# Kernel optimization log

Hardware: AMD Instinct MI355X
Metric: run time of the kernel (lower is better)

Reference implementation:

```python
import jax, jax.numpy as jnp
import numpy as np

NUM_HEADS = 4
B, C, N = 2, 128, 4096
NS = N // 2


def setup_inputs() -> dict:
    key = jax.random.key(0)
    ks = jax.random.split(key, 10)
    # idx_select/idx_drop together form a permutation of [0, N) per batch
    perms = jax.vmap(lambda k: jax.random.permutation(k, N))(jax.random.split(ks[8], B))
    idx_select = perms[:, :NS][:, None, :].astype(jnp.int64)
    idx_drop = perms[:, NS:][:, None, :].astype(jnp.int64)
    return {
        "pcd_up": jax.random.normal(ks[0], (B, C, N), jnp.float32),
        "points_select": jax.random.normal(ks[1], (B, C, NS), jnp.float32),
        "points_drop": jax.random.normal(ks[2], (B, C, NS), jnp.float32),
        "pcd_up_xyz": jax.random.normal(ks[3], (B, 3, N), jnp.float32),
        "Wq": jax.random.normal(ks[4], (C, C), jnp.float32) * 0.05,
        "Wk": jax.random.normal(ks[5], (C, C), jnp.float32) * 0.05,
        "Wv": jax.random.normal(ks[6], (C, C), jnp.float32) * 0.05,
        "Wskip": jax.random.normal(ks[7], (C, C), jnp.float32) * 0.05,
        "idx_select": idx_select,
        "idx_drop": idx_drop,
    }


def _concat_by_idx(a, b, idx_a, idx_b):
    # torch: target.scatter(-1, idx, cat([a,b],-1)) with idx expanded over channels
    src = jnp.concatenate([a, b], axis=-1)                  # [B, C, N]
    idx = jnp.concatenate([idx_a, idx_b], axis=-1)[:, 0, :]  # [B, N]
    return jax.vmap(lambda s, i: jnp.zeros_like(s).at[:, i].set(s))(src, idx)


def reference(pcd_up, points_select, points_drop, pcd_up_xyz, Wq, Wk, Wv, Wskip,
              idx_select, idx_drop):
    x = _concat_by_idx(points_select, points_drop, idx_select, idx_drop)  # [B,C,N]
    b, _, n = x.shape

    def proj_split(W, xx):
        y = jnp.einsum('oc,bcn->bon', W, xx)  # 1x1 Conv1d, no bias
        return y.reshape(b, NUM_HEADS, y.shape[1] // NUM_HEADS, n)  # [B,H,D,N]

    q = proj_split(Wq, x)
    k = proj_split(Wk, x)
    v = proj_split(Wv, x)
    dq = q.shape[2]
    # energy = q^T @ k, scaled by sqrt(q_depth)
    energy = jnp.einsum('bhdn,bhdm->bhnm', q, k) / jnp.sqrt(jnp.asarray(dq, x.dtype))
    attn = jax.nn.softmax(energy, axis=-1)                   # [B,H,N,N]
    out = jnp.einsum('bhnm,bhdm->bhnd', attn, v)             # [B,H,N,Dv]
    out = out.transpose(0, 2, 1, 3).reshape(b, n, -1).transpose(0, 2, 1)  # [B,v_out,N]
    return out + jnp.einsum('oc,bcn->bon', Wskip, pcd_up)
```

## Files before the change

### kernel.cpp

```cpp
#include <hip/hip_runtime.h>
#include <cstdint>

#define B_ 2
#define C_ 128
#define N_ 4096
#define H_ 4
#define D_ 32

typedef unsigned short ushort_t;
typedef __attribute__((ext_vector_type(8))) short bf16x8;
typedef __attribute__((ext_vector_type(4))) float f32x4;
typedef __attribute__((ext_vector_type(4))) unsigned int u32x4;

__device__ __forceinline__ ushort_t f2bf(float f) {
  unsigned int u = __builtin_bit_cast(unsigned int, f);
  u += 0x7fffu + ((u >> 16) & 1u);
  return (ushort_t)(u >> 16);
}

__device__ __forceinline__ void stage16(const ushort_t* g, ushort_t* l) {
  __builtin_amdgcn_global_load_lds(
      (const __attribute__((address_space(1))) unsigned int*)g,
      (__attribute__((address_space(3))) unsigned int*)l, 16, 0, 0);
}

__global__ __launch_bounds__(256) void k_prep(const float* __restrict__ psel,
                                              const float* __restrict__ pdrop,
                                              const int* __restrict__ isel,
                                              const int* __restrict__ idrop,
                                              const float* __restrict__ Wq,
                                              const float* __restrict__ Wk,
                                              const float* __restrict__ Wv,
                                              const float* __restrict__ Wsk,
                                              ushort_t* __restrict__ xT,
                                              ushort_t* __restrict__ Wb) {
  int z = blockIdx.z;
  int b = blockIdx.y;
  int t = threadIdx.x;
  {
    int gid = (((z * 2 + b) * 64 + blockIdx.x) << 8) + t;
    int m = gid >> 14, e = gid & 16383;
    const float* src = (m == 0) ? Wq : (m == 1) ? Wk : (m == 2) ? Wv : Wsk;
    float sc = (m == 0) ? 0.25506552f : 1.0f;
    Wb[m * 16384 + e] = f2bf(src[e] * sc);
  }
  const float* src = z ? pdrop : psel;
  const int* idx = z ? idrop : isel;
  __shared__ ushort_t tile[128][34];
  int i0 = blockIdx.x * 32;
  {
    int c = t >> 1, ih = (t & 1) * 16;
    const float4* p = (const float4*)(src + ((size_t)(b * 128 + c) * 2048 + i0 + ih));
#pragma unroll
    for (int g = 0; g < 4; ++g) {
      float4 v = p[g];
      tile[c][ih + g * 4 + 0] = f2bf(v.x);
      tile[c][ih + g * 4 + 1] = f2bf(v.y);
      tile[c][ih + g * 4 + 2] = f2bf(v.z);
      tile[c][ih + g * 4 + 3] = f2bf(v.w);
    }
  }
  __syncthreads();
  {
    int i = t >> 3, c0 = (t & 7) * 16;
    int n = idx[b * 2048 + i0 + i];
    alignas(16) ushort_t outv[16];
#pragma unroll
    for (int j = 0; j < 16; ++j) outv[j] = tile[c0 + j][i];
    uint4* q = (uint4*)(xT + ((size_t)(b * 4096 + n) * 128 + c0));
    q[0] = *(uint4*)outv; q[1] = *(uint4*)(outv + 8);
  }
}

__global__ __launch_bounds__(256) void k_proj(const ushort_t* __restrict__ xT,
                                              const ushort_t* __restrict__ Wb,
                                              ushort_t* __restrict__ Kb,
                                              ushort_t* __restrict__ Vt) {
  __shared__ float y[128][66];
  int n0 = blockIdx.x * 64, wt = blockIdx.y, b = blockIdx.z, t = threadIdx.x;
  int wave = t >> 6, lane = t & 63, lr = lane & 15, quad = lane >> 4;
  const ushort_t* W = Wb + (size_t)(wt + 1) * 16384;

  f32x4 acc[2][4];
#pragma unroll
  for (int mt = 0; mt < 2; ++mt)
#pragma unroll
    for (int nt = 0; nt < 4; ++nt) acc[mt][nt] = (f32x4){0.f, 0.f, 0.f, 0.f};
#pragma unroll
  for (int kc = 0; kc < 128; kc += 32) {
    bf16x8 a[2], bb[4];
#pragma unroll
    for (int mt = 0; mt < 2; ++mt)
      a[mt] = *(const bf16x8*)(W + (size_t)(wave * 32 + mt * 16 + lr) * 128 + kc + quad * 8);
#pragma unroll
    for (int nt = 0; nt < 4; ++nt)
      bb[nt] = *(const bf16x8*)(xT + ((size_t)(b * 4096 + n0 + nt * 16 + lr)) * 128 + kc + quad * 8);
#pragma unroll
    for (int mt = 0; mt < 2; ++mt)
#pragma unroll
      for (int nt = 0; nt < 4; ++nt)
        acc[mt][nt] = __builtin_amdgcn_mfma_f32_16x16x32_bf16(a[mt], bb[nt], acc[mt][nt], 0, 0, 0);
  }

#pragma unroll
  for (int mt = 0; mt < 2; ++mt)
#pragma unroll
    for (int nt = 0; nt < 4; ++nt)
#pragma unroll
      for (int r = 0; r < 4; ++r)
        y[wave * 32 + mt * 16 + quad * 4 + r][nt * 16 + lr] = acc[mt][nt][r];
  __syncthreads();

  if (wt == 0) {
    int n = t >> 2, dq = (t & 3) * 8;
#pragma unroll
    for (int h = 0; h < 4; ++h) {
      alignas(16) ushort_t vals[8];
#pragma unroll
      for (int j = 0; j < 8; ++j) vals[j] = f2bf(y[h * 32 + dq + j][n]);
      *(uint4*)(Kb + (((size_t)(b * 4 + h) * 4096 + n0 + n) * 32 + dq)) = *(uint4*)vals;
    }
  } else {
    int o = t >> 1, half = t & 1;
    int h = o >> 5, d = o & 31;
    alignas(16) ushort_t vals[32];
#pragma unroll
    for (int j = 0; j < 32; ++j) {
      int c = half * 32 + ((j >> 3) * 4 + (j & 3) + ((j & 4) << 2));
      vals[j] = f2bf(y[o][c]);
    }
    uint4* dst = (uint4*)(Vt + ((size_t)(b * 4 + h) * 32 + d) * 4096 + n0 + half * 32);
#pragma unroll
    for (int g = 0; g < 4; ++g) dst[g] = *(uint4*)(vals + g * 8);
  }
}

__global__ __launch_bounds__(1024) void k_attn(const ushort_t* __restrict__ xT,
                                               const float* __restrict__ pcd,
                                               const ushort_t* __restrict__ Wb,
                                               const ushort_t* __restrict__ Kb,
                                               const ushort_t* __restrict__ Vt,
                                               float* __restrict__ outp) {
  __shared__ ushort_t qT[4][32 * 40];
  __shared__ ushort_t stg[4][2][8192];

  int bh = blockIdx.x & 7;
  int q0 = (blockIdx.x >> 3) * 128;
  int b = bh >> 2, h = bh & 3;
  int t = threadIdx.x, wave = t >> 6, lane = t & 63, lr = lane & 15, quad = lane >> 4;
  int qh = wave & 3, kq = wave >> 2, lw = qh;
  int qbase = q0 + qh * 32;
  const ushort_t* xb = xT + (size_t)b * N_ * 128;
  const ushort_t* wqp = Wb + (size_t)h * 32 * 128;
  const ushort_t* Kp = Kb + (size_t)bh * N_ * 32;
  const ushort_t* Vp = Vt + (size_t)bh * 32 * N_;
  const int ks = kq * 1024;

#define STAGE_CHUNK(kcn, buf)                                                          \
  {                                                                                    \
    ushort_t* kb_ = stg[kq][buf];                                                      \
    ushort_t* vb_ = kb_ + 4096;                                                        \
    _Pragma("unroll") for (int j = 0; j < 2; ++j) {                                    \
      int s = lw * 2 + j;                                                              \
      stage16(Kp + (size_t)((kcn) + (s & 1) * 64 + lane) * 32 + (s >> 1) * 8,          \
              kb_ + s * 512);                                                          \
      int I = s * 64 + lane;                                                           \
      stage16(Vp + (size_t)(I & 31) * N_ + (kcn) + ((I >> 5) * 8), vb_ + s * 512);     \
    }                                                                                  \
  }

  if (kq == 0) {
    f32x4 accq[2][2];
#pragma unroll
    for (int mt = 0; mt < 2; ++mt)
#pragma unroll
      for (int nt = 0; nt < 2; ++nt) accq[mt][nt] = (f32x4){0.f, 0.f, 0.f, 0.f};
#pragma unroll
    for (int kc = 0; kc < 128; kc += 32) {
      bf16x8 ax[2], bw[2];
#pragma unroll
      for (int mt = 0; mt < 2; ++mt)
        ax[mt] = *(const bf16x8*)(xb + (size_t)(qbase + mt * 16 + lr) * 128 + kc + quad * 8);
#pragma unroll
      for (int nt = 0; nt < 2; ++nt)
        bw[nt] = *(const bf16x8*)(wqp + (size_t)(nt * 16 + lr) * 128 + kc + quad * 8);
#pragma unroll
      for (int mt = 0; mt < 2; ++mt)
#pragma unroll
        for (int nt = 0; nt < 2; ++nt)
          accq[mt][nt] = __builtin_amdgcn_mfma_f32_16x16x32_bf16(ax[mt], bw[nt], accq[mt][nt], 0, 0, 0);
    }
#pragma unroll
    for (int mt = 0; mt < 2; ++mt)
#pragma unroll
      for (int nt = 0; nt < 2; ++nt)
#pragma unroll
        for (int r = 0; r < 4; ++r)
          qT[qh][(mt * 16 + quad * 4 + r) * 40 + nt * 16 + lr] = f2bf(accq[mt][nt][r]);
  }

  STAGE_CHUNK(ks, 0);

  f32x4 accS[2][2];
#pragma unroll
  for (int mt = 0; mt < 2; ++mt)
#pragma unroll
    for (int nt = 0; nt < 2; ++nt) accS[mt][nt] = (f32x4){0.f, 0.f, 0.f, 0.f};
  if (kq == 1) {
    const ushort_t* wsk = Wb + 3 * 16384 + (size_t)h * 32 * 128;
#pragma unroll
    for (int kc = 0; kc < 128; kc += 32) {
      bf16x8 aS[2], bW[2];
#pragma unroll
      for (int mt = 0; mt < 2; ++mt) {
        alignas(16) ushort_t tmp[8];
#pragma unroll
        for (int j = 0; j < 8; ++j)
          tmp[j] = f2bf(pcd[((size_t)(b * 128 + kc + quad * 8 + j)) * 4096 + qbase + mt * 16 + lr]);
        aS[mt] = *(bf16x8*)tmp;
      }
#pragma unroll
      for (int nt = 0; nt < 2; ++nt)
        bW[nt] = *(const bf16x8*)(wsk + (size_t)(nt * 16 + lr) * 128 + kc + quad * 8);
#pragma unroll
      for (int mt = 0; mt < 2; ++mt)
#pragma unroll
        for (int nt = 0; nt < 2; ++nt)
          accS[mt][nt] = __builtin_amdgcn_mfma_f32_16x16x32_bf16(aS[mt], bW[nt], accS[mt][nt], 0, 0, 0);
    }
  }
  __syncthreads();

  bf16x8 aq0 = *(const bf16x8*)(&qT[qh][lr * 40 + quad * 8]);
  bf16x8 aq1 = *(const bf16x8*)(&qT[qh][(16 + lr) * 40 + quad * 8]);

  bf16x8 vones;
#pragma unroll
  for (int j = 0; j < 8; ++j) vones[j] = (short)0x3F80;

  f32x4 accO[2][2];
  f32x4 accR[2];
#pragma unroll
  for (int qf = 0; qf < 2; ++qf) {
#pragma unroll
    for (int dt = 0; dt < 2; ++dt) accO[qf][dt] = (f32x4){0.f, 0.f, 0.f, 0.f};
    accR[qf] = (f32x4){0.f, 0.f, 0.f, 0.f};
  }

  for (int it = 0; it < 8; ++it) {
    int cur = it & 1;
    if (it + 1 < 8) STAGE_CHUNK(ks + (it + 1) * 128, cur ^ 1);
    const ushort_t* kb = stg[kq][cur];
    const ushort_t* vb = kb + 4096;
#pragma unroll
    for (int g = 0; g < 4; ++g) {
      bf16x8 bk0 = *(const bf16x8*)(kb + (quad * 128 + g * 32 + lr) * 8);
      bf16x8 bk1 = *(const bf16x8*)(kb + (quad * 128 + g * 32 + 16 + lr) * 8);
      bf16x8 bv0 = *(const bf16x8*)(vb + ((g * 4 + quad) * 32 + lr) * 8);
      bf16x8 bv1 = *(const bf16x8*)(vb + ((g * 4 + quad) * 32 + 16 + lr) * 8);

      f32x4 z = {0.f, 0.f, 0.f, 0.f};
      f32x4 s0 = __builtin_amdgcn_mfma_f32_16x16x32_bf16(bk0, aq0, z, 0, 0, 0);
      f32x4 s1 = __builtin_amdgcn_mfma_f32_16x16x32_bf16(bk1, aq0, z, 0, 0, 0);
      f32x4 s2 = __builtin_amdgcn_mfma_f32_16x16x32_bf16(bk0, aq1, z, 0, 0, 0);
      f32x4 s3 = __builtin_amdgcn_mfma_f32_16x16x32_bf16(bk1, aq1, z, 0, 0, 0);
      float p0[4], p1[4], p2[4], p3[4];
#pragma unroll
      for (int r = 0; r < 4; ++r) {
        p0[r] = __builtin_amdgcn_exp2f(s0[r]);
        p1[r] = __builtin_amdgcn_exp2f(s1[r]);
        p2[r] = __builtin_amdgcn_exp2f(s2[r]);
        p3[r] = __builtin_amdgcn_exp2f(s3[r]);
      }
      u32x4 pk0, pk1;
      pk0.x = __builtin_amdgcn_perm(__builtin_bit_cast(unsigned int, p0[1]),
                                    __builtin_bit_cast(unsigned int, p0[0]), 0x07060302u);
      pk0.y = __builtin_amdgcn_perm(__builtin_bit_cast(unsigned int, p0[3]),
                                    __builtin_bit_cast(unsigned int, p0[2]), 0x07060302u);
      pk0.z = __builtin_amdgcn_perm(__builtin_bit_cast(unsigned int, p1[1]),
                                    __builtin_bit_cast(unsigned int, p1[0]), 0x07060302u);
      pk0.w = __builtin_amdgcn_perm(__builtin_bit_cast(unsigned int, p1[3]),
                                    __builtin_bit_cast(unsigned int, p1[2]), 0x07060302u);
      pk1.x = __builtin_amdgcn_perm(__builtin_bit_cast(unsigned int, p2[1]),
                                    __builtin_bit_cast(unsigned int, p2[0]), 0x07060302u);
      pk1.y = __builtin_amdgcn_perm(__builtin_bit_cast(unsigned int, p2[3]),
                                    __builtin_bit_cast(unsigned int, p2[2]), 0x07060302u);
      pk1.z = __builtin_amdgcn_perm(__builtin_bit_cast(unsigned int, p3[1]),
                                    __builtin_bit_cast(unsigned int, p3[0]), 0x07060302u);
      pk1.w = __builtin_amdgcn_perm(__builtin_bit_cast(unsigned int, p3[3]),
                                    __builtin_bit_cast(unsigned int, p3[2]), 0x07060302u);
      bf16x8 ap0 = __builtin_bit_cast(bf16x8, pk0);
      bf16x8 ap1 = __builtin_bit_cast(bf16x8, pk1);
      accO[0][0] = __builtin_amdgcn_mfma_f32_16x16x32_bf16(ap0, bv0, accO[0][0], 0, 0, 0);
      accO[0][1] = __builtin_amdgcn_mfma_f32_16x16x32_bf16(ap0, bv1, accO[0][1], 0, 0, 0);
      accO[1][0] = __builtin_amdgcn_mfma_f32_16x16x32_bf16(ap1, bv0, accO[1][0], 0, 0, 0);
      accO[1][1] = __builtin_amdgcn_mfma_f32_16x16x32_bf16(ap1, bv1, accO[1][1], 0, 0, 0);
      accR[0] = __builtin_amdgcn_mfma_f32_16x16x32_bf16(ap0, vones, accR[0], 0, 0, 0);
      accR[1] = __builtin_amdgcn_mfma_f32_16x16x32_bf16(ap1, vones, accR[1], 0, 0, 0);
    }
    __syncthreads();
  }

  float* pbuf = (float*)&stg[0][0][0];
  float* skipbuf = pbuf + 18432;
  float* obuf = pbuf + 22528;

  if (kq != 0) {
    float* pb = pbuf + (((kq - 1) * 4 + qh) * 64 + lane) * 24;
#pragma unroll
    for (int qf = 0; qf < 2; ++qf) {
#pragma unroll
      for (int dt = 0; dt < 2; ++dt)
#pragma unroll
        for (int r = 0; r < 4; ++r) pb[qf * 8 + dt * 4 + r] = accO[qf][dt][r];
#pragma unroll
      for (int r = 0; r < 4; ++r) pb[16 + qf * 4 + r] = accR[qf][r];
    }
    if (kq == 1) {
      float* sb = skipbuf + (qh * 64 + lane) * 16;
#pragma unroll
      for (int qf = 0; qf < 2; ++qf)
#pragma unroll
        for (int dt = 0; dt < 2; ++dt)
#pragma unroll
          for (int r = 0; r < 4; ++r) sb[qf * 8 + dt * 4 + r] = accS[qf][dt][r];
    }
  }
  __syncthreads();
  if (kq != 0) return;

#pragma unroll
  for (int j = 0; j < 3; ++j) {
    const float* pb = pbuf + ((j * 4 + qh) * 64 + lane) * 24;
#pragma unroll
    for (int qf = 0; qf < 2; ++qf) {
#pragma unroll
      for (int dt = 0; dt < 2; ++dt)
#pragma unroll
        for (int r = 0; r < 4; ++r) accO[qf][dt][r] += pb[qf * 8 + dt * 4 + r];
#pragma unroll
      for (int r = 0; r < 4; ++r) accR[qf][r] += pb[16 + qf * 4 + r];
    }
  }

  const float* sb = skipbuf + (qh * 64 + lane) * 16;
  float* ob = obuf + qh * 32 * 33;
#pragma unroll
  for (int qf = 0; qf < 2; ++qf) {
    float rinv[4];
#pragma unroll
    for (int r = 0; r < 4; ++r) rinv[r] = 1.0f / accR[qf][r];
#pragma unroll
    for (int dt = 0; dt < 2; ++dt)
#pragma unroll
      for (int r = 0; r < 4; ++r)
        ob[(dt * 16 + lr) * 33 + qf * 16 + quad * 4 + r] =
            accO[qf][dt][r] * rinv[r] + sb[qf * 8 + dt * 4 + r];
  }

  int d = lane >> 1, q16 = (lane & 1) * 16;
  float* po = outp + ((size_t)(b * 128 + h * 32 + d)) * N_ + qbase + q16;
#pragma unroll
  for (int g = 0; g < 4; ++g) {
    float4 r0;
    r0.x = ob[d * 33 + q16 + g * 4 + 0];
    r0.y = ob[d * 33 + q16 + g * 4 + 1];
    r0.z = ob[d * 33 + q16 + g * 4 + 2];
    r0.w = ob[d * 33 + q16 + g * 4 + 3];
    *(float4*)(po + g * 4) = r0;
  }
}

extern "C" void kernel_launch(void* const* d_in, const int* in_sizes, int n_in,
                              void* d_out, int out_size, void* d_ws, size_t ws_size,
                              hipStream_t stream) {
  const float* pcd_up = (const float*)d_in[0];
  const float* psel   = (const float*)d_in[1];
  const float* pdrop  = (const float*)d_in[2];
  const float* Wq  = (const float*)d_in[4];
  const float* Wk  = (const float*)d_in[5];
  const float* Wv  = (const float*)d_in[6];
  const float* Wsk = (const float*)d_in[7];
  const int* isel  = (const int*)d_in[8];
  const int* idrop = (const int*)d_in[9];
  float* out = (float*)d_out;

  ushort_t* xT = (ushort_t*)d_ws;
  ushort_t* Wb = xT + 1048576;
  ushort_t* Kb = Wb + 65536;
  ushort_t* Vt = Kb + 1048576;

  hipLaunchKernelGGL(k_prep, dim3(64, 2, 2), dim3(256), 0, stream,
                     psel, pdrop, isel, idrop, Wq, Wk, Wv, Wsk, xT, Wb);
  hipLaunchKernelGGL(k_proj, dim3(64, 2, 2), dim3(256), 0, stream, xT, Wb, Kb, Vt);
  hipLaunchKernelGGL(k_attn, dim3(256), dim3(1024), 0, stream,
                     xT, pcd_up, Wb, Kb, Vt, out);
}
```

Measured before the change: 113.4 us.

## Use per-wave private K/V staging and drop block-wide barriers in the attention loop

Before, each group of four query waves cooperatively staged 128-key K/V chunks into shared LDS and hit a block-wide __syncthreads every iteration. Now every wave stages its own 32-key chunk into a private double buffer and relies only on an s_waitcnt vmcnt wait, so waves no longer block one another. The loop runs 32 smaller iterations instead of 8. In exchange, the four waves with the same key range each fetch the same K/V data, raising global/L2 load traffic fourfold. The last iteration also issues a wrapped, unused prefetch.

```diff
diff --git a/kernel.cpp b/kernel.cpp
--- a/kernel.cpp
+++ b/kernel.cpp
@@ -142,31 +142,30 @@
                                                const ushort_t* __restrict__ Vt,
                                                float* __restrict__ outp) {
   __shared__ ushort_t qT[4][32 * 40];
-  __shared__ ushort_t stg[4][2][8192];
+  __shared__ ushort_t stg[16][2][2048];
 
   int bh = blockIdx.x & 7;
   int q0 = (blockIdx.x >> 3) * 128;
   int b = bh >> 2, h = bh & 3;
   int t = threadIdx.x, wave = t >> 6, lane = t & 63, lr = lane & 15, quad = lane >> 4;
-  int qh = wave & 3, kq = wave >> 2, lw = qh;
+  int qh = wave & 3, kq = wave >> 2;
   int qbase = q0 + qh * 32;
   const ushort_t* xb = xT + (size_t)b * N_ * 128;
   const ushort_t* wqp = Wb + (size_t)h * 32 * 128;
   const ushort_t* Kp = Kb + (size_t)bh * N_ * 32;
   const ushort_t* Vp = Vt + (size_t)bh * 32 * N_;
   const int ks = kq * 1024;
-
-#define STAGE_CHUNK(kcn, buf)                                                          \
-  {                                                                                    \
-    ushort_t* kb_ = stg[kq][buf];                                                      \
-    ushort_t* vb_ = kb_ + 4096;                                                        \
-    _Pragma("unroll") for (int j = 0; j < 2; ++j) {                                    \
-      int s = lw * 2 + j;                                                              \
-      stage16(Kp + (size_t)((kcn) + (s & 1) * 64 + lane) * 32 + (s >> 1) * 8,          \
-              kb_ + s * 512);                                                          \
-      int I = s * 64 + lane;                                                           \
-      stage16(Vp + (size_t)(I & 31) * N_ + (kcn) + ((I >> 5) * 8), vb_ + s * 512);     \
-    }                                                                                  \
+  int lk = lane & 31, lh = lane >> 5;
+
+#define STAGE_CHUNK(kcn, buf)                                                     \
+  {                                                                               \
+    ushort_t* kb_ = stg[wave][buf];                                               \
+    ushort_t* vb_ = kb_ + 1024;                                                   \
+    _Pragma("unroll") for (int s = 0; s < 2; ++s) {                               \
+      stage16(Kp + (size_t)((kcn) + lk) * 32 + (s * 2 + lh) * 8, kb_ + s * 512);  \
+      stage16(Vp + (size_t)lk * (size_t)N_ + (kcn) + (s * 2 + lh) * 8,            \
+              vb_ + s * 512);                                                     \
+    }                                                                             \
   }
 
   if (kq == 0) {
@@ -198,8 +197,6 @@
         for (int r = 0; r < 4; ++r)
           qT[qh][(mt * 16 + quad * 4 + r) * 40 + nt * 16 + lr] = f2bf(accq[mt][nt][r]);
   }
-
-  STAGE_CHUNK(ks, 0);
 
   f32x4 accS[2][2];
 #pragma unroll
@@ -229,6 +226,8 @@
           accS[mt][nt] = __builtin_amdgcn_mfma_f32_16x16x32_bf16(aS[mt], bW[nt], accS[mt][nt], 0, 0, 0);
     }
   }
+
+  STAGE_CHUNK(ks, 0);
   __syncthreads();
 
   bf16x8 aq0 = *(const bf16x8*)(&qT[qh][lr * 40 + quad * 8]);
@@ -247,64 +246,62 @@
     accR[qf] = (f32x4){0.f, 0.f, 0.f, 0.f};
   }
 
-  for (int it = 0; it < 8; ++it) {
+  for (int it = 0; it < 32; ++it) {
     int cur = it & 1;
-    if (it + 1 < 8) STAGE_CHUNK(ks + (it + 1) * 128, cur ^ 1);
-    const ushort_t* kb = stg[kq][cur];
-    const ushort_t* vb = kb + 4096;
-#pragma unroll
-    for (int g = 0; g < 4; ++g) {
-      bf16x8 bk0 = *(const bf16x8*)(kb + (quad * 128 + g * 32 + lr) * 8);
-      bf16x8 bk1 = *(const bf16x8*)(kb + (quad * 128 + g * 32 + 16 + lr) * 8);
-      bf16x8 bv0 = *(const bf16x8*)(vb + ((g * 4 + quad) * 32 + lr) * 8);
-      bf16x8 bv1 = *(const bf16x8*)(vb + ((g * 4 + quad) * 32 + 16 + lr) * 8);
-
-      f32x4 z = {0.f, 0.f, 0.f, 0.f};
-      f32x4 s0 = __builtin_amdgcn_mfma_f32_16x16x32_bf16(bk0, aq0, z, 0, 0, 0);
-      f32x4 s1 = __builtin_amdgcn_mfma_f32_16x16x32_bf16(bk1, aq0, z, 0, 0, 0);
-      f32x4 s2 = __builtin_amdgcn_mfma_f32_16x16x32_bf16(bk0, aq1, z, 0, 0, 0);
-      f32x4 s3 = __builtin_amdgcn_mfma_f32_16x16x32_bf16(bk1, aq1, z, 0, 0, 0);
-      float p0[4], p1[4], p2[4], p3[4];
-#pragma unroll
-      for (int r = 0; r < 4; ++r) {
-        p0[r] = __builtin_amdgcn_exp2f(s0[r]);
-        p1[r] = __builtin_amdgcn_exp2f(s1[r]);
-        p2[r] = __builtin_amdgcn_exp2f(s2[r]);
-        p3[r] = __builtin_amdgcn_exp2f(s3[r]);
-      }
-      u32x4 pk0, pk1;
-      pk0.x = __builtin_amdgcn_perm(__builtin_bit_cast(unsigned int, p0[1]),
-                                    __builtin_bit_cast(unsigned int, p0[0]), 0x07060302u);
-      pk0.y = __builtin_amdgcn_perm(__builtin_bit_cast(unsigned int, p0[3]),
-                                    __builtin_bit_cast(unsigned int, p0[2]), 0x07060302u);
-      pk0.z = __builtin_amdgcn_perm(__builtin_bit_cast(unsigned int, p1[1]),
-                                    __builtin_bit_cast(unsigned int, p1[0]), 0x07060302u);
-      pk0.w = __builtin_amdgcn_perm(__builtin_bit_cast(unsigned int, p1[3]),
-                                    __builtin_bit_cast(unsigned int, p1[2]), 0x07060302u);
-      pk1.x = __builtin_amdgcn_perm(__builtin_bit_cast(unsigned int, p2[1]),
-                                    __builtin_bit_cast(unsigned int, p2[0]), 0x07060302u);
-      pk1.y = __builtin_amdgcn_perm(__builtin_bit_cast(unsigned int, p2[3]),
-                                    __builtin_bit_cast(unsigned int, p2[2]), 0x07060302u);
-      pk1.z = __builtin_amdgcn_perm(__builtin_bit_cast(unsigned int, p3[1]),
-                                    __builtin_bit_cast(unsigned int, p3[0]), 0x07060302u);
-      pk1.w = __builtin_amdgcn_perm(__builtin_bit_cast(unsigned int, p3[3]),
-                                    __builtin_bit_cast(unsigned int, p3[2]), 0x07060302u);
-      bf16x8 ap0 = __builtin_bit_cast(bf16x8, pk0);
-      bf16x8 ap1 = __builtin_bit_cast(bf16x8, pk1);
-      accO[0][0] = __builtin_amdgcn_mfma_f32_16x16x32_bf16(ap0, bv0, accO[0][0], 0, 0, 0);
-      accO[0][1] = __builtin_amdgcn_mfma_f32_16x16x32_bf16(ap0, bv1, accO[0][1], 0, 0, 0);
-      accO[1][0] = __builtin_amdgcn_mfma_f32_16x16x32_bf16(ap1, bv0, accO[1][0], 0, 0, 0);
-      accO[1][1] = __builtin_amdgcn_mfma_f32_16x16x32_bf16(ap1, bv1, accO[1][1], 0, 0, 0);
-      accR[0] = __builtin_amdgcn_mfma_f32_16x16x32_bf16(ap0, vones, accR[0], 0, 0, 0);
-      accR[1] = __builtin_amdgcn_mfma_f32_16x16x32_bf16(ap1, vones, accR[1], 0, 0, 0);
-    }
-    __syncthreads();
+    STAGE_CHUNK(ks + (((it + 1) & 31) * 32), cur ^ 1);
+    asm volatile("s_waitcnt vmcnt(4)" ::: "memory");
+    const ushort_t* kb = stg[wave][cur];
+    const ushort_t* vb = kb + 1024;
+    bf16x8 bk0 = *(const bf16x8*)(kb + (quad >> 1) * 512 + (quad & 1) * 256 + lr * 8);
+    bf16x8 bk1 = *(const bf16x8*)(kb + (quad >> 1) * 512 + (quad & 1) * 256 + 128 + lr * 8);
+    bf16x8 bv0 = *(const bf16x8*)(vb + (quad * 32 + lr) * 8);
+    bf16x8 bv1 = *(const bf16x8*)(vb + (quad * 32 + 16 + lr) * 8);
+
+    f32x4 z = {0.f, 0.f, 0.f, 0.f};
+    f32x4 s0 = __builtin_amdgcn_mfma_f32_16x16x32_bf16(bk0, aq0, z, 0, 0, 0);
+    f32x4 s1 = __builtin_amdgcn_mfma_f32_16x16x32_bf16(bk1, aq0, z, 0, 0, 0);
+    f32x4 s2 = __builtin_amdgcn_mfma_f32_16x16x32_bf16(bk0, aq1, z, 0, 0, 0);
+    f32x4 s3 = __builtin_amdgcn_mfma_f32_16x16x32_bf16(bk1, aq1, z, 0, 0, 0);
+    float p0[4], p1[4], p2[4], p3[4];
+#pragma unroll
+    for (int r = 0; r < 4; ++r) {
+      p0[r] = __builtin_amdgcn_exp2f(s0[r]);
+      p1[r] = __builtin_amdgcn_exp2f(s1[r]);
+      p2[r] = __builtin_amdgcn_exp2f(s2[r]);
+      p3[r] = __builtin_amdgcn_exp2f(s3[r]);
+    }
+    u32x4 pk0, pk1;
+    pk0.x = __builtin_amdgcn_perm(__builtin_bit_cast(unsigned int, p0[1]),
+                                  __builtin_bit_cast(unsigned int, p0[0]), 0x07060302u);
+    pk0.y = __builtin_amdgcn_perm(__builtin_bit_cast(unsigned int, p0[3]),
+                                  __builtin_bit_cast(unsigned int, p0[2]), 0x07060302u);
+    pk0.z = __builtin_amdgcn_perm(__builtin_bit_cast(unsigned int, p1[1]),
+                                  __builtin_bit_cast(unsigned int, p1[0]), 0x07060302u);
+    pk0.w = __builtin_amdgcn_perm(__builtin_bit_cast(unsigned int, p1[3]),
+                                  __builtin_bit_cast(unsigned int, p1[2]), 0x07060302u);
+    pk1.x = __builtin_amdgcn_perm(__builtin_bit_cast(unsigned int, p2[1]),
+                                  __builtin_bit_cast(unsigned int, p2[0]), 0x07060302u);
+    pk1.y = __builtin_amdgcn_perm(__builtin_bit_cast(unsigned int, p2[3]),
+                                  __builtin_bit_cast(unsigned int, p2[2]), 0x07060302u);
+    pk1.z = __builtin_amdgcn_perm(__builtin_bit_cast(unsigned int, p3[1]),
+                                  __builtin_bit_cast(unsigned int, p3[0]), 0x07060302u);
+    pk1.w = __builtin_amdgcn_perm(__builtin_bit_cast(unsigned int, p3[3]),
+                                  __builtin_bit_cast(unsigned int, p3[2]), 0x07060302u);
+    bf16x8 ap0 = __builtin_bit_cast(bf16x8, pk0);
+    bf16x8 ap1 = __builtin_bit_cast(bf16x8, pk1);
+    accO[0][0] = __builtin_amdgcn_mfma_f32_16x16x32_bf16(ap0, bv0, accO[0][0], 0, 0, 0);
+    accO[0][1] = __builtin_amdgcn_mfma_f32_16x16x32_bf16(ap0, bv1, accO[0][1], 0, 0, 0);
+    accO[1][0] = __builtin_amdgcn_mfma_f32_16x16x32_bf16(ap1, bv0, accO[1][0], 0, 0, 0);
+    accO[1][1] = __builtin_amdgcn_mfma_f32_16x16x32_bf16(ap1, bv1, accO[1][1], 0, 0, 0);
+    accR[0] = __builtin_amdgcn_mfma_f32_16x16x32_bf16(ap0, vones, accR[0], 0, 0, 0);
+    accR[1] = __builtin_amdgcn_mfma_f32_16x16x32_bf16(ap1, vones, accR[1], 0, 0, 0);
   }
 
   float* pbuf = (float*)&stg[0][0][0];
   float* skipbuf = pbuf + 18432;
   float* obuf = pbuf + 22528;
 
+  __syncthreads();
   if (kq != 0) {
     float* pb = pbuf + (((kq - 1) * 4 + qh) * 64 + lane) * 24;
 #pragma unroll
```

New measurement: 135.1 us. 1.19x slower.
